# Kernel optimization log

Measured on AMD Instinct MI355X. Metric: run time of the kernel, lower is better.

## Reference

```python
import jax, jax.numpy as jnp
import numpy as np

LOG2 = float(np.log(2.0))

def ssp(x):
    # shifted softplus used by SchNet
    return jax.nn.softplus(x) - LOG2

def setup_inputs() -> dict:
    key = jax.random.key(0)
    k1, k2, k3, k4, k5 = jax.random.split(key, 5)
    N, E, D, F = 100000, 600000, 128, 64
    nodes = jax.random.normal(k1, (N, D), dtype=jnp.float32)
    edges = jax.random.normal(k2, (E, F), dtype=jnp.float32)
    edges_i = jax.random.randint(k3, (E, 2), 0, N, dtype=jnp.int64)
    W1 = jax.random.normal(k4, (F, D), dtype=jnp.float32) * (1.0 / np.sqrt(F))
    b1 = jnp.zeros((D,), dtype=jnp.float32)
    W2 = jax.random.normal(k5, (D, D), dtype=jnp.float32) * (1.0 / np.sqrt(D))
    b2 = jnp.zeros((D,), dtype=jnp.float32)
    return {"nodes": nodes, "edges": edges, "edges_i": edges_i,
            "W1": W1, "b1": b1, "W2": W2, "b2": b2}

def reference(nodes, edges, edges_i, W1, b1, W2, b2):
    starts = edges_i[:, 0]  # [E]
    ends = edges_i[:, 1]    # [E]
    # edge MLP filter: two Dense layers with shifted-softplus
    filt = ssp(edges @ W1 + b1)   # [E, D]
    filt = ssp(filt @ W2 + b2)    # [E, D]
    # gather end nodes, modulate by filter, scatter-add onto start nodes
    msgs = nodes[ends] * filt     # [E, D]
    return nodes.at[starts].add(msgs)  # [N, D]
```

## Files before the change

kernel.cpp:

```cpp
#include <hip/hip_runtime.h>
#include <math.h>

#define DD 128
#define FF 64
#define BM 64
#define SENT 0xFFFFFFFFu

typedef __attribute__((ext_vector_type(8))) short bf16x8;
typedef __attribute__((ext_vector_type(4))) short short4s;
typedef __attribute__((ext_vector_type(4))) float f32x4;

__device__ __forceinline__ float ssp_f(float x) {
    float ax = fabsf(x);
    float e  = __expf(-ax);
    return fmaxf(x, 0.0f) + __logf(1.0f + e) - 0.6931471805599453f;
}

__device__ __forceinline__ unsigned short f2bf(float f) {
    unsigned u = __float_as_uint(f);
    unsigned r = (u + 0x7FFFu + ((u >> 16) & 1u)) >> 16;
    return (unsigned short)r;
}
__device__ __forceinline__ float bf2f(unsigned short h) {
    return __uint_as_float(((unsigned)h) << 16);
}

__global__ void copy_nodes_kernel(const float4* __restrict__ src,
                                  float4* __restrict__ dst, int n4) {
    int i = blockIdx.x * blockDim.x + threadIdx.x;
    int stride = gridDim.x * blockDim.x;
    for (; i < n4; i += stride) dst[i] = src[i];
}

__global__ void zero_u32_kernel(unsigned* __restrict__ p, int n) {
    int i = blockIdx.x * blockDim.x + threadIdx.x;
    int stride = gridDim.x * blockDim.x;
    for (; i < n; i += stride) p[i] = 0u;
}

__global__ void hist_kernel(const int* __restrict__ eidx,
                            unsigned* __restrict__ counts, int E) {
    int e = blockIdx.x * blockDim.x + threadIdx.x;
    if (e < E) atomicAdd(&counts[eidx[2 * e]], 1u);
}

__global__ void scan1_kernel(const unsigned* __restrict__ counts,
                             unsigned* __restrict__ cursor,
                             unsigned* __restrict__ bsums, int n) {
    __shared__ unsigned s[256];
    int i = blockIdx.x * 256 + threadIdx.x;
    unsigned v = (i < n) ? counts[i] : 0u;
    s[threadIdx.x] = v;
    __syncthreads();
    #pragma unroll
    for (int d = 1; d < 256; d <<= 1) {
        unsigned t = (threadIdx.x >= d) ? s[threadIdx.x - d] : 0u;
        __syncthreads();
        s[threadIdx.x] += t;
        __syncthreads();
    }
    if (i < n) cursor[i] = s[threadIdx.x] - v;
    if (threadIdx.x == 255) bsums[blockIdx.x] = s[255];
}

__global__ void scan2_kernel(unsigned* __restrict__ bsums, int nb) {
    __shared__ unsigned s[512];
    int t = threadIdx.x;
    if (nb <= 512) {
        unsigned v = (t < nb) ? bsums[t] : 0u;
        s[t] = v;
        __syncthreads();
        #pragma unroll
        for (int d = 1; d < 512; d <<= 1) {
            unsigned x = (t >= d) ? s[t - d] : 0u;
            __syncthreads();
            s[t] += x;
            __syncthreads();
        }
        if (t < nb) bsums[t] = s[t] - v;
    } else if (t == 0) {
        unsigned run = 0u;
        for (int i = 0; i < nb; ++i) { unsigned x = bsums[i]; bsums[i] = run; run += x; }
    }
}

__global__ void scan3_kernel(unsigned* __restrict__ cursor,
                             const unsigned* __restrict__ bsums, int n) {
    int i = blockIdx.x * 256 + threadIdx.x;
    if (i < n) cursor[i] += bsums[blockIdx.x];
}

__global__ void scatter_move_kernel(const int* __restrict__ eidx,
                                    const float* __restrict__ edges,
                                    unsigned* __restrict__ cursor,
                                    unsigned short* __restrict__ edgesS,
                                    unsigned* __restrict__ sorted_nt,
                                    unsigned* __restrict__ sorted_ns, int E) {
    int e = blockIdx.x * blockDim.x + threadIdx.x;
    if (e >= E) return;
    int ns = eidx[2 * e];
    unsigned pos = atomicAdd(&cursor[ns], 1u);
    sorted_nt[pos] = (unsigned)eidx[2 * e + 1];
    sorted_ns[pos] = (unsigned)ns;

    int r = (int)(pos & 63);
    unsigned short* drow = edgesS + (size_t)pos * FF;
    const float4* src = reinterpret_cast<const float4*>(edges) + (size_t)e * 16;
    #pragma unroll
    for (int q = 0; q < 16; ++q) {
        float4 v = src[q];
        short4s hv = { (short)f2bf(v.x), (short)f2bf(v.y),
                       (short)f2bf(v.z), (short)f2bf(v.w) };
        int g = q >> 1, half = q & 1;
        *reinterpret_cast<short4s*>(drow + ((g ^ (r & 7)) * 8) + half * 4) = hv;
    }
}

__global__ void prep_w_kernel(const float* __restrict__ W, int K,
                              unsigned short* __restrict__ hi,
                              unsigned short* __restrict__ lo) {
    int S = K >> 5;
    int idx = blockIdx.x * blockDim.x + threadIdx.x;
    int total = 8 * S * 64;
    if (idx >= total) return;
    int l = idx & 63;
    int s = (idx >> 6) % S;
    int j = idx / (64 * S);
    int col = j * 16 + (l & 15);
    int kbase = s * 32 + (l >> 4) * 8;
    int ob = ((j * S + s) * 64 + l) * 8;
    #pragma unroll
    for (int i = 0; i < 8; ++i) {
        float w = W[(size_t)(kbase + i) * DD + col];
        unsigned short h = f2bf(w);
        hi[ob + i] = h;
        lo[ob + i] = f2bf(w - bf2f(h));
    }
}

__launch_bounds__(256, 4)
__global__ void edge_mfma_kernel(const float* __restrict__ nodes,
                                 const unsigned short* __restrict__ edgesS,
                                 const unsigned* __restrict__ sorted_nt,
                                 const unsigned* __restrict__ sorted_ns,
                                 const unsigned* __restrict__ ends,
                                 const unsigned short* __restrict__ W1h,
                                 const unsigned short* __restrict__ W1l,
                                 const unsigned short* __restrict__ W2h,
                                 const unsigned short* __restrict__ W2l,
                                 const float* __restrict__ b1,
                                 const float* __restrict__ b2,
                                 float* __restrict__ out,
                                 float* __restrict__ bpart,
                                 unsigned* __restrict__ bnode,
                                 int E) {
    __shared__ unsigned short region[16384];
    __shared__ float comm[128];
    float* SM = reinterpret_cast<float*>(region);

    const int t = threadIdx.x;
    const int tlo = blockIdx.x * BM;

    unsigned ns_reg = (tlo + (t & 63) < E) ? sorted_ns[tlo + (t & 63)] : SENT;

    {
        const bf16x8* src = reinterpret_cast<const bf16x8*>(edgesS + (size_t)tlo * FF);
        bf16x8* dst = reinterpret_cast<bf16x8*>(region);
        dst[t]       = src[t];
        dst[256 + t] = src[256 + t];
    }
    __syncthreads();

    const int lane = t & 63, wave = t >> 6;
    const int wrow = wave * 16;
    const int lr = lane & 15, lg = lane >> 4;
    const f32x4 zero4 = { 0.f, 0.f, 0.f, 0.f };

    bf16x8 a1[2];
    #pragma unroll
    for (int s = 0; s < 2; ++s) {
        int row = wrow + lr;
        a1[s] = *reinterpret_cast<const bf16x8*>(
            region + row * FF + (((s * 4 + lg) ^ (row & 7)) * 8));
    }
    __syncthreads();

    f32x4 acc1[8];
    #pragma unroll
    for (int j = 0; j < 8; ++j) acc1[j] = zero4;
    #pragma unroll
    for (int j = 0; j < 8; ++j) {
        bf16x8 wh[2], wl[2];
        #pragma unroll
        for (int s = 0; s < 2; ++s) {
            wh[s] = *reinterpret_cast<const bf16x8*>(W1h + ((size_t)((j * 2 + s) * 64 + lane)) * 8);
            wl[s] = *reinterpret_cast<const bf16x8*>(W1l + ((size_t)((j * 2 + s) * 64 + lane)) * 8);
        }
        #pragma unroll
        for (int s = 0; s < 2; ++s) {
            acc1[j] = __builtin_amdgcn_mfma_f32_16x16x32_bf16(a1[s], wh[s], acc1[j], 0, 0, 0);
            acc1[j] = __builtin_amdgcn_mfma_f32_16x16x32_bf16(a1[s], wl[s], acc1[j], 0, 0, 0);
        }
    }

    #pragma unroll
    for (int j = 0; j < 8; ++j) {
        int col = j * 16 + lr;
        float bv = b1[col];
        int gc = col >> 3, ci = col & 7;
        #pragma unroll
        for (int r = 0; r < 4; ++r) {
            int row = wrow + lg * 4 + r;
            region[row * DD + ((gc ^ (row & 15)) * 8 + ci)] =
                f2bf(ssp_f(acc1[j][r] + bv));
        }
    }
    __syncthreads();

    bf16x8 a2[4];
    #pragma unroll
    for (int s = 0; s < 4; ++s) {
        int row = wrow + lr;
        a2[s] = *reinterpret_cast<const bf16x8*>(
            region + row * DD + (((s * 4 + lg) ^ (row & 15)) * 8));
    }
    __syncthreads();

    float4 nv[8];
    const float4* n4 = reinterpret_cast<const float4*>(nodes);
    #pragma unroll
    for (int it = 0; it < 8; ++it) {
        int idx = it * 256 + t;
        int row = idx >> 5, c4 = idx & 31;
        unsigned nt_ = (tlo + row < E) ? sorted_nt[tlo + row] : 0u;
        nv[it] = n4[(size_t)nt_ * 32 + c4];
    }

    f32x4 acc2[8];
    #pragma unroll
    for (int j = 0; j < 8; ++j) acc2[j] = zero4;
    #pragma unroll
    for (int j = 0; j < 8; ++j) {
        bf16x8 wh[4], wl[4];
        #pragma unroll
        for (int s = 0; s < 4; ++s) {
            wh[s] = *reinterpret_cast<const bf16x8*>(W2h + ((size_t)((j * 4 + s) * 64 + lane)) * 8);
            wl[s] = *reinterpret_cast<const bf16x8*>(W2l + ((size_t)((j * 4 + s) * 64 + lane)) * 8);
        }
        #pragma unroll
        for (int s = 0; s < 4; ++s) {
            acc2[j] = __builtin_amdgcn_mfma_f32_16x16x32_bf16(a2[s], wh[s], acc2[j], 0, 0, 0);
            acc2[j] = __builtin_amdgcn_mfma_f32_16x16x32_bf16(a2[s], wl[s], acc2[j], 0, 0, 0);
        }
    }

    #pragma unroll
    for (int j = 0; j < 8; ++j) {
        int col = j * 16 + lr;
        float bv = b2[col];
        #pragma unroll
        for (int r = 0; r < 4; ++r) {
            int row = wrow + lg * 4 + r;
            SM[row * DD + (col ^ ((row & 7) << 2))] = ssp_f(acc2[j][r] + bv);
        }
    }
    __syncthreads();

    #pragma unroll
    for (int it = 0; it < 8; ++it) {
        int idx = it * 256 + t;
        int row = idx >> 5, c4 = idx & 31;
        int foff = row * DD + ((c4 * 4) ^ ((row & 7) << 2));
        float4 mv = *reinterpret_cast<float4*>(SM + foff);
        mv.x *= nv[it].x; mv.y *= nv[it].y; mv.z *= nv[it].z; mv.w *= nv[it].w;
        *reinterpret_cast<float4*>(SM + foff) = mv;
    }
    __syncthreads();

    {
        int pl = (lane == 0) ? 0 : lane - 1;
        unsigned prevns = __shfl(ns_reg, pl);
        unsigned long long bnd = __ballot((lane > 0) && (ns_reg != prevns));

        unsigned n0  = __shfl(ns_reg, 0);
        unsigned n31 = __shfl(ns_reg, 31);
        unsigned n32 = __shfl(ns_reg, 32);
        bool cont_mid = (n31 == n32) && (n31 != SENT);
        unsigned s0 = (n0 == 0u) ? 0u : ends[n0 - 1];
        bool contFirst = (s0 < (unsigned)tlo);
        bool spans0 = (n0 == n31);

        const int y = t >> 7;
        const int col = t & 127;
        const int rbeg = y * 32;

        float firstacc = 0.f;
        bool firstpend = false;

        float acc = 0.f;
        int segstart = rbeg;
        bool pend = (y == 1) && cont_mid;
        #pragma unroll 1
        for (int r = rbeg; r < rbeg + 32; ++r) {
            if (r > rbeg && ((bnd >> r) & 1ull)) {
                unsigned node = __shfl(ns_reg, segstart);
                if (pend) {
                    firstacc = acc; firstpend = true; pend = false;
                } else if (node != SENT) {
                    if (segstart == 0 && contFirst)
                        bpart[(size_t)blockIdx.x * DD + col] = acc;
                    else
                        out[(size_t)node * DD + col] = nodes[(size_t)node * DD + col] + acc;
                }
                acc = 0.f; segstart = r;
            }
            acc += SM[r * DD + (col ^ ((r & 7) << 2))];
        }
        {
            unsigned node = __shfl(ns_reg, segstart);
            if (y == 0 && cont_mid) {
                comm[col] = acc;
            } else if (pend) {
                firstacc = acc; firstpend = true;
            } else if (node != SENT) {
                if (segstart == 0 && contFirst)
                    bpart[(size_t)blockIdx.x * DD + col] = acc;
                else
                    out[(size_t)node * DD + col] = nodes[(size_t)node * DD + col] + acc;
            }
        }
        if (t == 0) bnode[blockIdx.x] = contFirst ? n0 : SENT;
        __syncthreads();

        if (y == 1 && firstpend) {
            float total = comm[col] + firstacc;
            if (spans0 && contFirst)
                bpart[(size_t)blockIdx.x * DD + col] = total;
            else
                out[(size_t)n31 * DD + col] = nodes[(size_t)n31 * DD + col] + total;
        }
    }
}

__global__ void fixup_bpart_kernel(const float* __restrict__ bpart,
                                   const unsigned* __restrict__ bnode,
                                   float* __restrict__ out, int NT) {
    int ti = blockIdx.x * 2 + (threadIdx.x >> 7);
    if (ti >= NT) return;
    unsigned n = bnode[ti];
    if (n == SENT) return;
    int c = threadIdx.x & 127;
    atomicAdd(&out[(size_t)n * DD + c], bpart[(size_t)ti * DD + c]);
}

__global__ void copy_empty_kernel(const unsigned* __restrict__ counts,
                                  const float4* __restrict__ nodes4,
                                  float4* __restrict__ out4, int N) {
    int n = blockIdx.x * 8 + (threadIdx.x >> 5);
    if (n >= N) return;
    if (counts[n] != 0u) return;
    int d4 = threadIdx.x & 31;
    out4[(size_t)n * 32 + d4] = nodes4[(size_t)n * 32 + d4];
}

__launch_bounds__(256, 2)
__global__ void edge_fused_atomic_kernel(const float* __restrict__ nodes,
                                         const float* __restrict__ edges,
                                         const int*   __restrict__ eidx,
                                         const float* __restrict__ W1,
                                         const float* __restrict__ b1,
                                         const float* __restrict__ W2,
                                         const float* __restrict__ b2,
                                         float* __restrict__ out, int E) {
    int e = blockIdx.x * 256 + threadIdx.x;
    if (e >= E) return;
    int ns = eidx[2 * e + 0];
    int nt = eidx[2 * e + 1];

    float h1[DD];
    #pragma unroll
    for (int d = 0; d < DD; ++d) h1[d] = b1[d];
    const float4* ev4 = reinterpret_cast<const float4*>(edges) + (size_t)e * (FF / 4);
    #pragma unroll 1
    for (int f4 = 0; f4 < FF / 4; ++f4) {
        float4 ev = ev4[f4];
        const float* w0 = W1 + (size_t)(f4 * 4) * DD;
        #pragma unroll
        for (int d = 0; d < DD; ++d) h1[d] = fmaf(ev.x, w0[d], h1[d]);
        #pragma unroll
        for (int d = 0; d < DD; ++d) h1[d] = fmaf(ev.y, w0[DD + d], h1[d]);
        #pragma unroll
        for (int d = 0; d < DD; ++d) h1[d] = fmaf(ev.z, w0[2 * DD + d], h1[d]);
        #pragma unroll
        for (int d = 0; d < DD; ++d) h1[d] = fmaf(ev.w, w0[3 * DD + d], h1[d]);
    }
    #pragma unroll
    for (int d = 0; d < DD; ++d) h1[d] = ssp_f(h1[d]);

    const float* nrow = nodes + (size_t)nt * DD;
    float*       orow = out   + (size_t)ns * DD;
    #pragma unroll 1
    for (int c = 0; c < 2; ++c) {
        const int base = c * 64;
        float h2[64];
        #pragma unroll
        for (int j = 0; j < 64; ++j) h2[j] = b2[base + j];
        #pragma unroll
        for (int k = 0; k < DD; ++k) {
            float hk = h1[k];
            const float* w = W2 + (size_t)k * DD + base;
            #pragma unroll
            for (int j = 0; j < 64; ++j) h2[j] = fmaf(hk, w[j], h2[j]);
        }
        #pragma unroll
        for (int j = 0; j < 64; ++j) {
            float m = ssp_f(h2[j]) * nrow[base + j];
            __hip_atomic_fetch_add(&orow[base + j], m,
                                   __ATOMIC_RELAXED, __HIP_MEMORY_SCOPE_AGENT);
        }
    }
}

extern "C" void kernel_launch(void* const* d_in, const int* in_sizes, int n_in,
                              void* d_out, int out_size, void* d_ws, size_t ws_size,
                              hipStream_t stream) {
    const float* nodes = (const float*)d_in[0];
    const float* edges = (const float*)d_in[1];
    const int*   eidx  = (const int*)  d_in[2];
    const float* W1    = (const float*)d_in[3];
    const float* b1    = (const float*)d_in[4];
    const float* W2    = (const float*)d_in[5];
    const float* b2    = (const float*)d_in[6];
    float* out = (float*)d_out;

    int ND = in_sizes[0];
    int N  = ND / DD;
    int E  = in_sizes[1] / FF;
    int NT = (E + BM - 1) / BM;

    int nb = (N + 255) / 256;
    uintptr_t base = (uintptr_t)d_ws;
    uintptr_t p = base;
    unsigned* counts    = (unsigned*)p;  p += (size_t)N * 4;
    unsigned* cursor    = (unsigned*)p;  p += (size_t)N * 4;
    unsigned* bsums     = (unsigned*)p;  p += (size_t)nb * 4;
    unsigned* sorted_nt = (unsigned*)p;  p += (size_t)E * 4;
    unsigned* sorted_ns = (unsigned*)p;  p += (size_t)E * 4;
    p = (p + 255) & ~(uintptr_t)255;
    unsigned short* W1h = (unsigned short*)p;  p += (size_t)FF * DD * 2;
    unsigned short* W1l = (unsigned short*)p;  p += (size_t)FF * DD * 2;
    unsigned short* W2h = (unsigned short*)p;  p += (size_t)DD * DD * 2;
    unsigned short* W2l = (unsigned short*)p;  p += (size_t)DD * DD * 2;
    unsigned* bnode     = (unsigned*)p;  p += (size_t)NT * 4;
    p = (p + 255) & ~(uintptr_t)255;
    float* bpart        = (float*)p;     p += (size_t)NT * DD * 4;
    p = (p + 255) & ~(uintptr_t)255;
    unsigned short* edgesS = (unsigned short*)p;
    p += (size_t)NT * BM * FF * 2;

    if ((size_t)(p - base) > ws_size) {
        copy_nodes_kernel<<<dim3(1024), dim3(256), 0, stream>>>(
            (const float4*)nodes, (float4*)out, ND / 4);
        edge_fused_atomic_kernel<<<dim3((E + 255) / 256), dim3(256), 0, stream>>>(
            nodes, edges, eidx, W1, b1, W2, b2, out, E);
        return;
    }

    prep_w_kernel<<<dim3(4), dim3(256), 0, stream>>>(W1, FF, W1h, W1l);
    prep_w_kernel<<<dim3(8), dim3(256), 0, stream>>>(W2, DD, W2h, W2l);

    zero_u32_kernel<<<dim3(256), dim3(256), 0, stream>>>(counts, N);
    hist_kernel<<<dim3((E + 255) / 256), dim3(256), 0, stream>>>(eidx, counts, E);
    scan1_kernel<<<dim3(nb), dim3(256), 0, stream>>>(counts, cursor, bsums, N);
    scan2_kernel<<<dim3(1), dim3(512), 0, stream>>>(bsums, nb);
    scan3_kernel<<<dim3(nb), dim3(256), 0, stream>>>(cursor, bsums, N);
    scatter_move_kernel<<<dim3((E + 255) / 256), dim3(256), 0, stream>>>(
        eidx, edges, cursor, edgesS, sorted_nt, sorted_ns, E);

    copy_empty_kernel<<<dim3((N + 7) / 8), dim3(256), 0, stream>>>(
        counts, (const float4*)nodes, (float4*)out, N);

    edge_mfma_kernel<<<dim3(NT), dim3(256), 0, stream>>>(
        nodes, edgesS, sorted_nt, sorted_ns, cursor,
        W1h, W1l, W2h, W2l, b1, b2, out, bpart, bnode, E);

    fixup_bpart_kernel<<<dim3((NT + 1) / 2), dim3(256), 0, stream>>>(
        bpart, bnode, out, NT);
}
```

Baseline: 381.0 us.

## Split second GEMM and scatter into two column halves to halve LDS

The second dense layer, the node-gather multiply and the segmented reduction now run in two passes over 64-column halves. This lets the shared staging buffer shrink to half its size, and the launch bound rises from 4 to 5 blocks per SIMD to gain occupancy. In exchange it adds extra barriers and runs the reduction on only 128 threads per pass, which serializes more work. The tighter launch bound may also force register spills.

```diff
diff --git a/kernel.cpp b/kernel.cpp
--- a/kernel.cpp
+++ b/kernel.cpp
@@ -138,7 +138,7 @@
     }
 }
 
-__launch_bounds__(256, 4)
+__launch_bounds__(256, 5)
 __global__ void edge_mfma_kernel(const float* __restrict__ nodes,
                                  const unsigned short* __restrict__ edgesS,
                                  const unsigned* __restrict__ sorted_nt,
@@ -154,8 +154,8 @@
                                  float* __restrict__ bpart,
                                  unsigned* __restrict__ bnode,
                                  int E) {
-    __shared__ unsigned short region[16384];
-    __shared__ float comm[128];
+    __shared__ unsigned short region[8192];
+    __shared__ float comm[64];
     float* SM = reinterpret_cast<float*>(region);
 
     const int t = threadIdx.x;
@@ -226,114 +226,122 @@
     }
     __syncthreads();
 
-    float4 nv[8];
-    const float4* n4 = reinterpret_cast<const float4*>(nodes);
-    #pragma unroll
-    for (int it = 0; it < 8; ++it) {
-        int idx = it * 256 + t;
-        int row = idx >> 5, c4 = idx & 31;
-        unsigned nt_ = (tlo + row < E) ? sorted_nt[tlo + row] : 0u;
-        nv[it] = n4[(size_t)nt_ * 32 + c4];
-    }
-
-    f32x4 acc2[8];
-    #pragma unroll
-    for (int j = 0; j < 8; ++j) acc2[j] = zero4;
-    #pragma unroll
-    for (int j = 0; j < 8; ++j) {
-        bf16x8 wh[4], wl[4];
-        #pragma unroll
-        for (int s = 0; s < 4; ++s) {
-            wh[s] = *reinterpret_cast<const bf16x8*>(W2h + ((size_t)((j * 4 + s) * 64 + lane)) * 8);
-            wl[s] = *reinterpret_cast<const bf16x8*>(W2l + ((size_t)((j * 4 + s) * 64 + lane)) * 8);
-        }
-        #pragma unroll
-        for (int s = 0; s < 4; ++s) {
-            acc2[j] = __builtin_amdgcn_mfma_f32_16x16x32_bf16(a2[s], wh[s], acc2[j], 0, 0, 0);
-            acc2[j] = __builtin_amdgcn_mfma_f32_16x16x32_bf16(a2[s], wl[s], acc2[j], 0, 0, 0);
-        }
-    }
-
-    #pragma unroll
-    for (int j = 0; j < 8; ++j) {
-        int col = j * 16 + lr;
-        float bv = b2[col];
-        #pragma unroll
-        for (int r = 0; r < 4; ++r) {
-            int row = wrow + lg * 4 + r;
-            SM[row * DD + (col ^ ((row & 7) << 2))] = ssp_f(acc2[j][r] + bv);
-        }
-    }
-    __syncthreads();
-
-    #pragma unroll
-    for (int it = 0; it < 8; ++it) {
-        int idx = it * 256 + t;
-        int row = idx >> 5, c4 = idx & 31;
-        int foff = row * DD + ((c4 * 4) ^ ((row & 7) << 2));
-        float4 mv = *reinterpret_cast<float4*>(SM + foff);
-        mv.x *= nv[it].x; mv.y *= nv[it].y; mv.z *= nv[it].z; mv.w *= nv[it].w;
-        *reinterpret_cast<float4*>(SM + foff) = mv;
-    }
-    __syncthreads();
-
-    {
-        int pl = (lane == 0) ? 0 : lane - 1;
-        unsigned prevns = __shfl(ns_reg, pl);
-        unsigned long long bnd = __ballot((lane > 0) && (ns_reg != prevns));
-
-        unsigned n0  = __shfl(ns_reg, 0);
-        unsigned n31 = __shfl(ns_reg, 31);
-        unsigned n32 = __shfl(ns_reg, 32);
-        bool cont_mid = (n31 == n32) && (n31 != SENT);
-        unsigned s0 = (n0 == 0u) ? 0u : ends[n0 - 1];
-        bool contFirst = (s0 < (unsigned)tlo);
-        bool spans0 = (n0 == n31);
-
-        const int y = t >> 7;
-        const int col = t & 127;
-        const int rbeg = y * 32;
+    int pl = (lane == 0) ? 0 : lane - 1;
+    unsigned prevns = __shfl(ns_reg, pl);
+    unsigned long long bnd = __ballot((lane > 0) && (ns_reg != prevns));
+    unsigned n0  = __shfl(ns_reg, 0);
+    unsigned n31 = __shfl(ns_reg, 31);
+    unsigned n32 = __shfl(ns_reg, 32);
+    bool cont_mid = (n31 == n32) && (n31 != SENT);
+    unsigned s0 = (n0 == 0u) ? 0u : ends[n0 - 1];
+    bool contFirst = (s0 < (unsigned)tlo);
+    bool spans0 = (n0 == n31);
+
+    const float4* n4p = reinterpret_cast<const float4*>(nodes);
+
+    #pragma unroll 1
+    for (int h = 0; h < 2; ++h) {
+        float4 nv[4];
+        #pragma unroll
+        for (int it = 0; it < 4; ++it) {
+            int idx = it * 256 + t;
+            int row = idx >> 4, c4 = idx & 15;
+            unsigned nt_ = (tlo + row < E) ? sorted_nt[tlo + row] : 0u;
+            nv[it] = n4p[(size_t)nt_ * 32 + h * 16 + c4];
+        }
+
+        f32x4 acc2[4];
+        #pragma unroll
+        for (int jj = 0; jj < 4; ++jj) acc2[jj] = zero4;
+        #pragma unroll
+        for (int jj = 0; jj < 4; ++jj) {
+            int j = h * 4 + jj;
+            bf16x8 wh[4], wl[4];
+            #pragma unroll
+            for (int s = 0; s < 4; ++s) {
+                wh[s] = *reinterpret_cast<const bf16x8*>(W2h + ((size_t)((j * 4 + s) * 64 + lane)) * 8);
+                wl[s] = *reinterpret_cast<const bf16x8*>(W2l + ((size_t)((j * 4 + s) * 64 + lane)) * 8);
+            }
+            #pragma unroll
+            for (int s = 0; s < 4; ++s) {
+                acc2[jj] = __builtin_amdgcn_mfma_f32_16x16x32_bf16(a2[s], wh[s], acc2[jj], 0, 0, 0);
+                acc2[jj] = __builtin_amdgcn_mfma_f32_16x16x32_bf16(a2[s], wl[s], acc2[jj], 0, 0, 0);
+            }
+        }
+
+        #pragma unroll
+        for (int jj = 0; jj < 4; ++jj) {
+            int col = (h * 4 + jj) * 16 + lr;
+            float bv = b2[col];
+            int colh = jj * 16 + lr;
+            #pragma unroll
+            for (int r = 0; r < 4; ++r) {
+                int row = wrow + lg * 4 + r;
+                SM[row * 64 + (colh ^ (((row >> 2) & 3) << 4))] =
+                    ssp_f(acc2[jj][r] + bv);
+            }
+        }
+        __syncthreads();
+
+        #pragma unroll
+        for (int it = 0; it < 4; ++it) {
+            int idx = it * 256 + t;
+            int row = idx >> 4, c4 = idx & 15;
+            int foff = row * 64 + ((c4 * 4) ^ (((row >> 2) & 3) << 4));
+            float4 mv = *reinterpret_cast<float4*>(SM + foff);
+            mv.x *= nv[it].x; mv.y *= nv[it].y; mv.z *= nv[it].z; mv.w *= nv[it].w;
+            *reinterpret_cast<float4*>(SM + foff) = mv;
+        }
+        __syncthreads();
 
         float firstacc = 0.f;
         bool firstpend = false;
-
-        float acc = 0.f;
-        int segstart = rbeg;
-        bool pend = (y == 1) && cont_mid;
-        #pragma unroll 1
-        for (int r = rbeg; r < rbeg + 32; ++r) {
-            if (r > rbeg && ((bnd >> r) & 1ull)) {
+        if (t < 128) {
+            const int y = t >> 6;
+            const int colh = t & 63;
+            const int col = h * 64 + colh;
+            const int rbeg = y * 32;
+
+            float acc = 0.f;
+            int segstart = rbeg;
+            bool pend = (y == 1) && cont_mid;
+            #pragma unroll 1
+            for (int r = rbeg; r < rbeg + 32; ++r) {
+                if (r > rbeg && ((bnd >> r) & 1ull)) {
+                    unsigned node = __shfl(ns_reg, segstart);
+                    if (pend) {
+                        firstacc = acc; firstpend = true; pend = false;
+                    } else if (node != SENT) {
+                        if (segstart == 0 && contFirst)
+                            bpart[(size_t)blockIdx.x * DD + col] = acc;
+                        else
+                            out[(size_t)node * DD + col] = nodes[(size_t)node * DD + col] + acc;
+                    }
+                    acc = 0.f; segstart = r;
+                }
+                acc += SM[r * 64 + (colh ^ (((r >> 2) & 3) << 4))];
+            }
+            {
                 unsigned node = __shfl(ns_reg, segstart);
-                if (pend) {
-                    firstacc = acc; firstpend = true; pend = false;
+                if (y == 0 && cont_mid) {
+                    comm[colh] = acc;
+                } else if (pend) {
+                    firstacc = acc; firstpend = true;
                 } else if (node != SENT) {
                     if (segstart == 0 && contFirst)
                         bpart[(size_t)blockIdx.x * DD + col] = acc;
                     else
                         out[(size_t)node * DD + col] = nodes[(size_t)node * DD + col] + acc;
                 }
-                acc = 0.f; segstart = r;
             }
-            acc += SM[r * DD + (col ^ ((r & 7) << 2))];
-        }
-        {
-            unsigned node = __shfl(ns_reg, segstart);
-            if (y == 0 && cont_mid) {
-                comm[col] = acc;
-            } else if (pend) {
-                firstacc = acc; firstpend = true;
-            } else if (node != SENT) {
-                if (segstart == 0 && contFirst)
-                    bpart[(size_t)blockIdx.x * DD + col] = acc;
-                else
-                    out[(size_t)node * DD + col] = nodes[(size_t)node * DD + col] + acc;
-            }
-        }
-        if (t == 0) bnode[blockIdx.x] = contFirst ? n0 : SENT;
-        __syncthreads();
-
-        if (y == 1 && firstpend) {
-            float total = comm[col] + firstacc;
+            if (t == 0 && h == 0) bnode[blockIdx.x] = contFirst ? n0 : SENT;
+        }
+        __syncthreads();
+
+        if (t >= 64 && t < 128 && firstpend) {
+            const int colh = t & 63;
+            const int col = h * 64 + colh;
+            float total = comm[colh] + firstacc;
             if (spans0 && contFirst)
                 bpart[(size_t)blockIdx.x * DD + col] = total;
             else
```

After: 536.3 us. 40.8% more time.
